# Performance work log

Measured on AMD Instinct MI355X. Metric: run time of the kernel, lower is better.

The kernel has to match this reference:

```python
import jax, jax.numpy as jnp
import numpy as np

NB = 8  # num_blocks

def setup_inputs() -> dict:
    key = jax.random.key(0)
    ks = jax.random.split(key, 8)
    C = 128
    C8 = C // 8
    s = 0.05
    x = jax.random.normal(ks[0], (1, C, 64, 64, 64), dtype=jnp.float32)
    Wq = jax.random.normal(ks[1], (C8, C), dtype=jnp.float32) * s
    bq = jax.random.normal(ks[2], (C8,), dtype=jnp.float32) * s
    Wk = jax.random.normal(ks[3], (C8, C), dtype=jnp.float32) * s
    bk = jax.random.normal(ks[4], (C8,), dtype=jnp.float32) * s
    Wv = jax.random.normal(ks[5], (C, C), dtype=jnp.float32) * s
    bv = jax.random.normal(ks[6], (C,), dtype=jnp.float32) * s
    # torch inits gamma=0 (output == x, zero grads through attention);
    # use 0.5 so the attention path is actually exercised.
    gamma = jnp.full((1,), 0.5, dtype=jnp.float32)
    return dict(x=x, Wq=Wq, bq=bq, Wk=Wk, bk=bk, Wv=Wv, bv=bv, gamma=gamma)

def reference(x, Wq, bq, Wk, bk, Wv, bv, gamma):
    B, C, D, H, W = x.shape
    db, hb, wb = D // NB, H // NB, W // NB
    n = db * hb * wb
    # (i, j, k, B, C, db, hb, wb) block layout
    xr = x.reshape(B, C, NB, db, NB, hb, NB, wb).transpose(2, 4, 6, 0, 1, 3, 5, 7)
    ar = jnp.arange(NB)
    # NOTE: original code computes k = i % num_blocks, i.e. k == i always.
    # Only the (i, j, i) diagonal blocks are attended; the rest stay zero in `out`.
    blk = xr[ar, :, ar].reshape(NB * NB * B, C, n)  # (P, C, n), P = NB*NB*B
    # 1x1x1 convs == per-voxel linear layers over channels
    q = jnp.einsum('pcn,dc->pdn', blk, Wq) + bq[None, :, None]  # (P, C/8, n)
    k = jnp.einsum('pcn,dc->pdn', blk, Wk) + bk[None, :, None]  # (P, C/8, n)
    v = jnp.einsum('pcn,dc->pdn', blk, Wv) + bv[None, :, None]  # (P, C,   n)
    attn = jax.nn.softmax(jnp.einsum('pdn,pdm->pnm', q, k), axis=-1)  # (P, n_q, n_k)
    ob = jnp.einsum('pdm,pnm->pdn', v, attn)  # value @ attn^T, (P, C, n)
    ob = ob.reshape(NB, NB, B, C, db, hb, wb)
    out = jnp.zeros_like(xr).at[ar, :, ar].set(ob)  # only k==i diagonal filled
    out = out.transpose(3, 4, 0, 5, 1, 6, 2, 7).reshape(B, C, D, H, W)
    return gamma * out + x
```

## Files before the change

kernel.cpp:

```cpp
#include <hip/hip_runtime.h>

typedef __attribute__((ext_vector_type(8))) short bf16x8;
typedef __attribute__((ext_vector_type(4))) float f32x4;
typedef __attribute__((ext_vector_type(4))) int i32x4;
typedef __attribute__((ext_vector_type(4))) float float4v;

#define MFMA16(a, b, c) __builtin_amdgcn_mfma_f32_16x16x32_bf16((a), (b), (c), 0, 0, 0)

__device__ __forceinline__ unsigned short f2bf(float f) {
    unsigned u = __builtin_bit_cast(unsigned, f);
    u += 0x7fffu + ((u >> 16) & 1u);
    return (unsigned short)(u >> 16);
}
__device__ __forceinline__ float bf2f(unsigned short s) {
    unsigned u = ((unsigned)s) << 16;
    return __builtin_bit_cast(float, u);
}
__device__ __forceinline__ int pkbf(float a, float b) {
    return (int)f2bf(a) | ((int)f2bf(b) << 16);
}

#define KOFF 131072
#define LOFF 147456

__global__ __launch_bounds__(512, 2) void battn_kernel(
    const float* __restrict__ x,
    const float* __restrict__ Wq, const float* __restrict__ bq,
    const float* __restrict__ Wk, const float* __restrict__ bk,
    const float* __restrict__ Wv, const float* __restrict__ bv,
    const float* __restrict__ gamma, float* __restrict__ out)
{
    __shared__ __attribute__((aligned(128))) char smem[147968];
    const int tid = threadIdx.x;
    const int bid = blockIdx.x;
    const int p  = ((bid & 7) << 3) | (bid >> 5);
    const int qq = (bid >> 3) & 3;
    const int ib = p >> 3, jb = p & 7;
    const int vbase = ib * 8 * 4096 + jb * 8 * 64 + ib * 8;
    const int lane = tid & 63, wv = tid >> 6;
    const int g = lane >> 4, c15 = lane & 15;

    #pragma unroll
    for (int b = 0; b < 4; ++b) {
        float4v t[8];
        #pragma unroll
        for (int j = 0; j < 8; ++j) {
            int ch = (b * 8 + j) * 512 + tid;
            int c = ch >> 7;
            int m = (ch & 127) * 4;
            int vox = ((m >> 6) << 12) + (((m >> 3) & 7) << 6) + (m & 7);
            t[j] = *(const float4v*)(x + c * 262144 + vbase + vox);
        }
        #pragma unroll
        for (int j = 0; j < 8; ++j) {
            int ch = (b * 8 + j) * 512 + tid;
            int c = ch >> 7;
            int m = (ch & 127) * 4;
            char* bp = smem + ((m * 256 + 2 * c) ^ (((m >> 2) & 7) << 4));
            *(unsigned short*)(bp)       = f2bf(t[j][0]);
            *(unsigned short*)(bp + 256) = f2bf(t[j][1]);
            *(unsigned short*)(bp + 512) = f2bf(t[j][2]);
            *(unsigned short*)(bp + 768) = f2bf(t[j][3]);
        }
    }

    bf16x8 wqf[4], wkf[4], wvf[4];
    #pragma unroll
    for (int ks = 0; ks < 4; ++ks) {
        const float4v* sq = (const float4v*)(Wq + c15 * 128 + ks * 32 + g * 8);
        const float4v* sk = (const float4v*)(Wk + c15 * 128 + ks * 32 + g * 8);
        const float4v* sv = (const float4v*)(Wv + (wv * 16 + c15) * 128 + ks * 32 + g * 8);
        float4v q0 = sq[0], q1 = sq[1];
        float4v k0 = sk[0], k1 = sk[1];
        float4v v0 = sv[0], v1 = sv[1];
        #pragma unroll
        for (int e = 0; e < 4; ++e) {
            wqf[ks][e] = (short)f2bf(q0[e]); wqf[ks][4 + e] = (short)f2bf(q1[e]);
            wkf[ks][e] = (short)f2bf(k0[e]); wkf[ks][4 + e] = (short)f2bf(k1[e]);
            wvf[ks][e] = (short)f2bf(v0[e]); wvf[ks][4 + e] = (short)f2bf(v1[e]);
        }
    }
    const float bqv = bq[c15], bkv = bk[c15];
    const f32x4 zacc = {0.f, 0.f, 0.f, 0.f};
    const bf16x8 zfrag = (bf16x8)(short)0;

    __syncthreads();

    {
        f32x4 acc = zacc;
        int mrow = qq * 128 + wv * 16 + c15;
        int sw = ((mrow >> 2) & 7) << 4;
        #pragma unroll
        for (int ks = 0; ks < 4; ++ks) {
            bf16x8 af = *(const bf16x8*)(smem + ((mrow * 256 + ks * 64 + g * 16) ^ sw));
            acc = MFMA16(af, wqf[ks], acc);
        }
        #pragma unroll
        for (int r = 0; r < 4; ++r)
            *(unsigned short*)(smem + KOFF + wv * 2048 + (g * 4 + r) * 32 + 2 * c15) = f2bf(acc[r] + bqv);
    }
    bf16x8 qf = zfrag;
    if (g < 2) qf = *(const bf16x8*)(smem + KOFF + wv * 2048 + c15 * 32 + g * 16);

    #pragma unroll
    for (int qi = 0; qi < 4; ++qi) {
        f32x4 acc = zacc;
        int mrow = wv * 64 + qi * 16 + c15;
        int sw = ((mrow >> 2) & 7) << 4;
        #pragma unroll
        for (int ks = 0; ks < 4; ++ks) {
            bf16x8 af = *(const bf16x8*)(smem + ((mrow * 256 + ks * 64 + g * 16) ^ sw));
            acc = MFMA16(af, wkf[ks], acc);
        }
        #pragma unroll
        for (int r = 0; r < 4; ++r) {
            int mk = wv * 64 + qi * 16 + g * 4 + r;
            *(unsigned short*)(smem + KOFF + mk * 32 + 2 * c15) = f2bf(acc[r] + bkv);
        }
    }

    for (int ck = 0; ck < 4; ++ck) {
        f32x4 vacc[8];
        #pragma unroll
        for (int mt = 0; mt < 8; ++mt) {
            vacc[mt] = zacc;
            int mrow = ck * 128 + mt * 16 + c15;
            int sw = ((mrow >> 2) & 7) << 4;
            #pragma unroll
            for (int ks = 0; ks < 4; ++ks) {
                bf16x8 bf = *(const bf16x8*)(smem + ((mrow * 256 + ks * 64 + g * 16) ^ sw));
                vacc[mt] = MFMA16(wvf[ks], bf, vacc[mt]);
            }
        }
        __syncthreads();
        #pragma unroll
        for (int mt = 0; mt < 8; ++mt) {
            #pragma unroll
            for (int r = 0; r < 4; ++r) {
                int c_out = wv * 16 + g * 4 + r;
                int mkl = mt * 16 + c15;
                *(unsigned short*)(smem + ck * 32768 + c_out * 256 +
                                   ((2 * mkl) ^ ((c_out & 7) << 4))) = f2bf(vacc[mt][r]);
            }
        }
    }
    __syncthreads();

    f32x4 o[8];
    #pragma unroll
    for (int ci = 0; ci < 8; ++ci) o[ci] = zacc;
    float lsum = 0.f;

    for (int kt = 0; kt < 16; ++kt) {
        int mk0 = kt * 32;
        bf16x8 ka[2];
        #pragma unroll
        for (int ki = 0; ki < 2; ++ki) {
            bf16x8 v = zfrag;
            if (g < 2) v = *(const bf16x8*)(smem + KOFF + (mk0 + ki * 16 + c15) * 32 + g * 16);
            ka[ki] = v;
        }

        f32x4 s0 = MFMA16(ka[0], qf, zacc);
        f32x4 s1 = MFMA16(ka[1], qf, zacc);
        float e00 = __expf(s0[0]), e01 = __expf(s0[1]), e02 = __expf(s0[2]), e03 = __expf(s0[3]);
        float e10 = __expf(s1[0]), e11 = __expf(s1[1]), e12 = __expf(s1[2]), e13 = __expf(s1[3]);
        lsum += (e00 + e01) + (e02 + e03) + ((e10 + e11) + (e12 + e13));
        int wA0 = pkbf(e00, e01), wB0 = pkbf(e02, e03);
        int wA1 = pkbf(e10, e11), wB1 = pkbf(e12, e13);
        int src1 = ((2 * g) & 3) * 16 + c15;
        int src2 = ((2 * g + 1) & 3) * 16 + c15;
        int sA0a = __shfl(wA0, src1, 64), sA1a = __shfl(wA1, src1, 64);
        int sB0a = __shfl(wB0, src1, 64), sB1a = __shfl(wB1, src1, 64);
        int sA0b = __shfl(wA0, src2, 64), sA1b = __shfl(wA1, src2, 64);
        int sB0b = __shfl(wB0, src2, 64), sB1b = __shfl(wB1, src2, 64);
        bool k1 = (g >= 2);
        i32x4 uu = { k1 ? sA1a : sA0a, k1 ? sB1a : sB0a,
                     k1 ? sA1b : sA0b, k1 ? sB1b : sB0b };
        bf16x8 pa = __builtin_bit_cast(bf16x8, uu);

        int ckbase = (mk0 >> 7) * 32768;
        int mklb = (2 * (mk0 & 127)) + 16 * g;
        #pragma unroll
        for (int ci = 0; ci < 8; ++ci) {
            int c = ci * 16 + c15;
            bf16x8 vb = *(const bf16x8*)(smem + ckbase + c * 256 + (mklb ^ ((c & 7) << 4)));
            o[ci] = MFMA16(pa, vb, o[ci]);
        }
    }

    {
        float l = lsum;
        l += __shfl_xor(l, 16, 64);
        l += __shfl_xor(l, 32, 64);
        if (g == 0)
            *(float*)(smem + LOFF + (wv * 16 + c15) * 4) = l;
    }

    __syncthreads();

    #pragma unroll
    for (int ci = 0; ci < 8; ++ci)
        #pragma unroll
        for (int r = 0; r < 4; ++r) {
            int nql = wv * 16 + g * 4 + r;
            int c = ci * 16 + c15;
            *(unsigned short*)(smem + c * 256 + ((2 * nql) ^ ((c & 7) << 4))) = f2bf(o[ci][r]);
        }
    __syncthreads();

    float gma = gamma[0];
    int q128 = tid & 127;
    int cb = tid >> 7;
    float invl = 1.0f / *(const float*)(smem + LOFF + q128 * 4);
    int nq = qq * 128 + q128;
    int vox = ((nq >> 6) << 12) + (((nq >> 3) & 7) << 6) + (nq & 7);
    int go = vbase + vox;
    #pragma unroll
    for (int b = 0; b < 4; ++b) {
        float xv[8];
        #pragma unroll
        for (int j = 0; j < 8; ++j) {
            int c = cb * 32 + b * 8 + j;
            xv[j] = x[c * 262144 + go];
        }
        #pragma unroll
        for (int j = 0; j < 8; ++j) {
            int c = cb * 32 + b * 8 + j;
            float ov = bf2f(*(const unsigned short*)(smem + c * 256 + ((2 * q128) ^ ((c & 7) << 4))));
            out[c * 262144 + go] = gma * (ov * invl + bv[c]) + xv[j];
        }
    }
}

extern "C" void kernel_launch(void* const* d_in, const int* in_sizes, int n_in,
                              void* d_out, int out_size, void* d_ws, size_t ws_size,
                              hipStream_t stream) {
    const float* x     = (const float*)d_in[0];
    const float* Wq    = (const float*)d_in[1];
    const float* bq    = (const float*)d_in[2];
    const float* Wk    = (const float*)d_in[3];
    const float* bk    = (const float*)d_in[4];
    const float* Wv    = (const float*)d_in[5];
    const float* bv    = (const float*)d_in[6];
    const float* gamma = (const float*)d_in[7];
    float* out = (float*)d_out;
    (void)in_sizes; (void)n_in; (void)out_size; (void)d_ws; (void)ws_size;

    hipMemcpyAsync(out, x, (size_t)out_size * sizeof(float),
                   hipMemcpyDeviceToDevice, stream);
    battn_kernel<<<dim3(256), dim3(512), 0, stream>>>(x, Wq, bq, Wk, bk, Wv, bv, gamma, out);
}
```

Measured before the change: 101.1 us.

## Pre-gather diagonal blocks into contiguous workspace before attention kernel

Adds a separate gather kernel that copies the strided diagonal 8x8x8 voxel blocks of x into a contiguous per-block workspace layout. The attention kernel then reads its input tile and residual values from that workspace with coalesced vector loads instead of scattered strided reads. The trade-off is an extra kernel launch and an extra round trip of the gathered data through memory. Each attention block re-reads its tile four times (once per query quarter), so cheaper reads may outweigh the added traffic.

New measurement: 123.8 us. 22.4% more time.

```diff
diff --git a/kernel.cpp b/kernel.cpp
--- a/kernel.cpp
+++ b/kernel.cpp
@@ -20,11 +20,29 @@
     return (int)f2bf(a) | ((int)f2bf(b) << 16);
 }
 
+__global__ __launch_bounds__(512) void gather_kernel(
+    const float* __restrict__ x, float* __restrict__ ws)
+{
+    int gid = blockIdx.x * 512 + threadIdx.x;
+    int gm = gid & 63;
+    int c  = (gid >> 6) & 127;
+    int p  = gid >> 13;
+    int ib = p >> 3, jb = p & 7;
+    int dd = gm >> 3, hh = gm & 7;
+    const float* src = x + c * 262144 + ib * 32768 + jb * 512 + ib * 8
+                         + dd * 4096 + hh * 64;
+    float4v a0 = *(const float4v*)(src);
+    float4v a1 = *(const float4v*)(src + 4);
+    float* dst = ws + (size_t)gid * 8;
+    *(float4v*)(dst)     = a0;
+    *(float4v*)(dst + 4) = a1;
+}
+
 #define KOFF 131072
 #define LOFF 147456
 
 __global__ __launch_bounds__(512, 2) void battn_kernel(
-    const float* __restrict__ x,
+    const float* __restrict__ ws,
     const float* __restrict__ Wq, const float* __restrict__ bq,
     const float* __restrict__ Wk, const float* __restrict__ bk,
     const float* __restrict__ Wv, const float* __restrict__ bv,
@@ -39,23 +57,19 @@
     const int vbase = ib * 8 * 4096 + jb * 8 * 64 + ib * 8;
     const int lane = tid & 63, wv = tid >> 6;
     const int g = lane >> 4, c15 = lane & 15;
+    const float4v* __restrict__ wsp4 = (const float4v*)(ws + p * 65536);
 
     #pragma unroll
     for (int b = 0; b < 4; ++b) {
         float4v t[8];
         #pragma unroll
+        for (int j = 0; j < 8; ++j)
+            t[j] = wsp4[(b * 8 + j) * 512 + tid];
+        #pragma unroll
         for (int j = 0; j < 8; ++j) {
-            int ch = (b * 8 + j) * 512 + tid;
-            int c = ch >> 7;
-            int m = (ch & 127) * 4;
-            int vox = ((m >> 6) << 12) + (((m >> 3) & 7) << 6) + (m & 7);
-            t[j] = *(const float4v*)(x + c * 262144 + vbase + vox);
-        }
-        #pragma unroll
-        for (int j = 0; j < 8; ++j) {
-            int ch = (b * 8 + j) * 512 + tid;
-            int c = ch >> 7;
-            int m = (ch & 127) * 4;
+            int u = (b * 8 + j) * 512 + tid;
+            int c = u >> 7;
+            int m = (u & 127) * 4;
             char* bp = smem + ((m * 256 + 2 * c) ^ (((m >> 2) & 7) << 4));
             *(unsigned short*)(bp)       = f2bf(t[j][0]);
             *(unsigned short*)(bp + 256) = f2bf(t[j][1]);
@@ -216,13 +230,14 @@
     int nq = qq * 128 + q128;
     int vox = ((nq >> 6) << 12) + (((nq >> 3) & 7) << 6) + (nq & 7);
     int go = vbase + vox;
+    const float* wsr = ws + p * 65536 + nq;
     #pragma unroll
     for (int b = 0; b < 4; ++b) {
         float xv[8];
         #pragma unroll
         for (int j = 0; j < 8; ++j) {
             int c = cb * 32 + b * 8 + j;
-            xv[j] = x[c * 262144 + go];
+            xv[j] = wsr[c * 512];
         }
         #pragma unroll
         for (int j = 0; j < 8; ++j) {
@@ -245,9 +260,11 @@
     const float* bv    = (const float*)d_in[6];
     const float* gamma = (const float*)d_in[7];
     float* out = (float*)d_out;
-    (void)in_sizes; (void)n_in; (void)out_size; (void)d_ws; (void)ws_size;
+    float* ws  = (float*)d_ws;
+    (void)in_sizes; (void)n_in; (void)out_size; (void)ws_size;
 
     hipMemcpyAsync(out, x, (size_t)out_size * sizeof(float),
                    hipMemcpyDeviceToDevice, stream);
-    battn_kernel<<<dim3(256), dim3(512), 0, stream>>>(x, Wq, bq, Wk, bk, Wv, bv, gamma, out);
-}
+    gather_kernel<<<dim3(1024), dim3(512), 0, stream>>>(x, ws);
+    battn_kernel<<<dim3(256), dim3(512), 0, stream>>>(ws, Wq, bq, Wk, bk, Wv, bv, gamma, out);
+}
```

## Split projection into separate kernel writing Q/K/V to workspace

Applied to the files above, without the earlier changes.

The fused kernel made each of the four query-quarter blocks redundantly recompute the full K and V projections for its attention block. A new proj_kernel computes Q, K and V once per block, split across 8 CTAs, and writes them as bf16 to the workspace along with a contiguous fp32 copy of x. The attention kernel then loads precomputed K and V into shared memory and reads the residual from the contiguous copy. This removes redundant MFMA work and raises parallelism in the projection phase, at the cost of an extra launch and extra workspace traffic.

New measurement: 115.7 us. 1.14x slower.

```diff
diff --git a/kernel.cpp b/kernel.cpp
--- a/kernel.cpp
+++ b/kernel.cpp
@@ -1,6 +1,7 @@
 #include <hip/hip_runtime.h>
 
 typedef __attribute__((ext_vector_type(8))) short bf16x8;
+typedef __attribute__((ext_vector_type(8))) unsigned short u16x8;
 typedef __attribute__((ext_vector_type(4))) float f32x4;
 typedef __attribute__((ext_vector_type(4))) int i32x4;
 typedef __attribute__((ext_vector_type(4))) float float4v;
@@ -20,15 +21,149 @@
     return (int)f2bf(a) | ((int)f2bf(b) << 16);
 }
 
-#define KOFF 131072
-#define LOFF 147456
-
-__global__ __launch_bounds__(512, 2) void battn_kernel(
+
+__global__ __launch_bounds__(256, 4) void proj_kernel(
     const float* __restrict__ x,
     const float* __restrict__ Wq, const float* __restrict__ bq,
     const float* __restrict__ Wk, const float* __restrict__ bk,
-    const float* __restrict__ Wv, const float* __restrict__ bv,
-    const float* __restrict__ gamma, float* __restrict__ out)
+    const float* __restrict__ Wv,
+    float* __restrict__ ws)
+{
+    __shared__ __attribute__((aligned(128))) char smem[36864];
+    const int tid = threadIdx.x;
+    const int bid = blockIdx.x;
+    const int p = bid >> 3, s = bid & 7;
+    const int ib = p >> 3, jb = p & 7;
+    const int vbase = ib * 32768 + jb * 512 + ib * 8;
+    const int lane = tid & 63, wv = tid >> 6;
+    const int g = lane >> 4, c15 = lane & 15;
+    const f32x4 zacc = {0.f, 0.f, 0.f, 0.f};
+
+    bf16x8 wqf[4], wkf[4], wvf2[2][4];
+    #pragma unroll
+    for (int ks = 0; ks < 4; ++ks) {
+        const float4v* sq = (const float4v*)(Wq + c15 * 128 + ks * 32 + g * 8);
+        const float4v* sk = (const float4v*)(Wk + c15 * 128 + ks * 32 + g * 8);
+        float4v q0 = sq[0], q1 = sq[1];
+        float4v k0 = sk[0], k1 = sk[1];
+        #pragma unroll
+        for (int e = 0; e < 4; ++e) {
+            wqf[ks][e] = (short)f2bf(q0[e]); wqf[ks][4 + e] = (short)f2bf(q1[e]);
+            wkf[ks][e] = (short)f2bf(k0[e]); wkf[ks][4 + e] = (short)f2bf(k1[e]);
+        }
+        #pragma unroll
+        for (int cg = 0; cg < 2; ++cg) {
+            const float4v* sv = (const float4v*)(Wv + (wv * 32 + cg * 16 + c15) * 128 + ks * 32 + g * 8);
+            float4v v0 = sv[0], v1 = sv[1];
+            #pragma unroll
+            for (int e = 0; e < 4; ++e) {
+                wvf2[cg][ks][e] = (short)f2bf(v0[e]); wvf2[cg][ks][4 + e] = (short)f2bf(v1[e]);
+            }
+        }
+    }
+    const float bqv = bq[c15], bkv = bk[c15];
+
+    float* blkws = ws + p * 65536;
+    #pragma unroll
+    for (int k = 0; k < 2; ++k) {
+        int pi = k * 256 + tid;
+        int cpair = pi >> 3, m8 = pi & 7;
+        int c0 = cpair * 2;
+        int mg = s * 64 + m8 * 8;
+        int vox = s * 4096 + m8 * 64;
+        const float* src0 = x + c0 * 262144 + vbase + vox;
+        float4v a0 = *(const float4v*)(src0);
+        float4v a1 = *(const float4v*)(src0 + 4);
+        float4v b0 = *(const float4v*)(src0 + 262144);
+        float4v b1 = *(const float4v*)(src0 + 262144 + 4);
+        *(float4v*)(blkws + c0 * 512 + mg)           = a0;
+        *(float4v*)(blkws + c0 * 512 + mg + 4)       = a1;
+        *(float4v*)(blkws + c0 * 512 + 512 + mg)     = b0;
+        *(float4v*)(blkws + c0 * 512 + 512 + mg + 4) = b1;
+        int ml = m8 * 8;
+        #pragma unroll
+        for (int j = 0; j < 4; ++j) {
+            int m = ml + j;
+            unsigned v = (unsigned)f2bf(a0[j]) | ((unsigned)f2bf(b0[j]) << 16);
+            *(unsigned*)(smem + ((m * 256 + 4 * cpair) ^ (((m >> 2) & 7) << 4))) = v;
+        }
+        #pragma unroll
+        for (int j = 0; j < 4; ++j) {
+            int m = ml + 4 + j;
+            unsigned v = (unsigned)f2bf(a1[j]) | ((unsigned)f2bf(b1[j]) << 16);
+            *(unsigned*)(smem + ((m * 256 + 4 * cpair) ^ (((m >> 2) & 7) << 4))) = v;
+        }
+    }
+    __syncthreads();
+
+    {
+        f32x4 qa = zacc, kacc = zacc;
+        int mrow = wv * 16 + c15;
+        int sw = ((mrow >> 2) & 7) << 4;
+        #pragma unroll
+        for (int ks = 0; ks < 4; ++ks) {
+            bf16x8 af = *(const bf16x8*)(smem + ((mrow * 256 + ks * 64 + g * 16) ^ sw));
+            qa = MFMA16(af, wqf[ks], qa);
+            kacc = MFMA16(af, wkf[ks], kacc);
+        }
+        #pragma unroll
+        for (int r = 0; r < 4; ++r) {
+            int row = wv * 16 + g * 4 + r;
+            *(unsigned short*)(smem + 16384 + row * 32 + 2 * c15) = f2bf(qa[r] + bqv);
+            *(unsigned short*)(smem + 18432 + row * 32 + 2 * c15) = f2bf(kacc[r] + bkv);
+        }
+    }
+
+    f32x4 vacc[2][4];
+    #pragma unroll
+    for (int cg = 0; cg < 2; ++cg)
+        #pragma unroll
+        for (int mt = 0; mt < 4; ++mt) {
+            vacc[cg][mt] = zacc;
+            int mrow = mt * 16 + c15;
+            int sw = ((mrow >> 2) & 7) << 4;
+            #pragma unroll
+            for (int ks = 0; ks < 4; ++ks) {
+                bf16x8 bf = *(const bf16x8*)(smem + ((mrow * 256 + ks * 64 + g * 16) ^ sw));
+                vacc[cg][mt] = MFMA16(wvf2[cg][ks], bf, vacc[cg][mt]);
+            }
+        }
+    char* vt = smem + 20480 + wv * 4096;
+    #pragma unroll
+    for (int cg = 0; cg < 2; ++cg)
+        #pragma unroll
+        for (int mt = 0; mt < 4; ++mt)
+            #pragma unroll
+            for (int r = 0; r < 4; ++r)
+                *(unsigned short*)(vt + (cg * 16 + g * 4 + r) * 128 + 2 * (mt * 16 + c15))
+                    = f2bf(vacc[cg][mt][r]);
+
+    unsigned short* wsh = (unsigned short*)(ws + 4194304);
+    unsigned short* wsv = wsh + 1048576 + p * 65536 + s * 64;
+    #pragma unroll
+    for (int i = 0; i < 4; ++i) {
+        int lb = i * 1024 + lane * 16;
+        u16x8 vv = *(const u16x8*)(vt + lb);
+        int c_local = lb >> 7;
+        int moff = (lane & 7) * 8;
+        *(u16x8*)(wsv + (wv * 32 + c_local) * 512 + moff) = vv;
+    }
+    __syncthreads();
+    unsigned short* wsq = wsh + p * 8192 + s * 1024;
+    unsigned short* wsk = wsh + 524288 + p * 8192 + s * 1024;
+    long long qd = *(const long long*)(smem + 16384 + tid * 8);
+    long long kd = *(const long long*)(smem + 18432 + tid * 8);
+    *(long long*)(wsq + tid * 4) = qd;
+    *(long long*)(wsk + tid * 4) = kd;
+}
+
+#define KOFF 131072
+#define LOFF 147456
+
+__global__ __launch_bounds__(512, 2) void attn_kernel(
+    const float* __restrict__ ws,
+    const float* __restrict__ bv, const float* __restrict__ gamma,
+    float* __restrict__ out)
 {
     __shared__ __attribute__((aligned(128))) char smem[147968];
     const int tid = threadIdx.x;
@@ -36,114 +171,32 @@
     const int p  = ((bid & 7) << 3) | (bid >> 5);
     const int qq = (bid >> 3) & 3;
     const int ib = p >> 3, jb = p & 7;
-    const int vbase = ib * 8 * 4096 + jb * 8 * 64 + ib * 8;
+    const int vbase = ib * 32768 + jb * 512 + ib * 8;
     const int lane = tid & 63, wv = tid >> 6;
     const int g = lane >> 4, c15 = lane & 15;
-
-    #pragma unroll
-    for (int b = 0; b < 4; ++b) {
-        float4v t[8];
-        #pragma unroll
-        for (int j = 0; j < 8; ++j) {
-            int ch = (b * 8 + j) * 512 + tid;
-            int c = ch >> 7;
-            int m = (ch & 127) * 4;
-            int vox = ((m >> 6) << 12) + (((m >> 3) & 7) << 6) + (m & 7);
-            t[j] = *(const float4v*)(x + c * 262144 + vbase + vox);
-        }
-        #pragma unroll
-        for (int j = 0; j < 8; ++j) {
-            int ch = (b * 8 + j) * 512 + tid;
-            int c = ch >> 7;
-            int m = (ch & 127) * 4;
-            char* bp = smem + ((m * 256 + 2 * c) ^ (((m >> 2) & 7) << 4));
-            *(unsigned short*)(bp)       = f2bf(t[j][0]);
-            *(unsigned short*)(bp + 256) = f2bf(t[j][1]);
-            *(unsigned short*)(bp + 512) = f2bf(t[j][2]);
-            *(unsigned short*)(bp + 768) = f2bf(t[j][3]);
-        }
-    }
-
-    bf16x8 wqf[4], wkf[4], wvf[4];
-    #pragma unroll
-    for (int ks = 0; ks < 4; ++ks) {
-        const float4v* sq = (const float4v*)(Wq + c15 * 128 + ks * 32 + g * 8);
-        const float4v* sk = (const float4v*)(Wk + c15 * 128 + ks * 32 + g * 8);
-        const float4v* sv = (const float4v*)(Wv + (wv * 16 + c15) * 128 + ks * 32 + g * 8);
-        float4v q0 = sq[0], q1 = sq[1];
-        float4v k0 = sk[0], k1 = sk[1];
-        float4v v0 = sv[0], v1 = sv[1];
-        #pragma unroll
-        for (int e = 0; e < 4; ++e) {
-            wqf[ks][e] = (short)f2bf(q0[e]); wqf[ks][4 + e] = (short)f2bf(q1[e]);
-            wkf[ks][e] = (short)f2bf(k0[e]); wkf[ks][4 + e] = (short)f2bf(k1[e]);
-            wvf[ks][e] = (short)f2bf(v0[e]); wvf[ks][4 + e] = (short)f2bf(v1[e]);
-        }
-    }
-    const float bqv = bq[c15], bkv = bk[c15];
     const f32x4 zacc = {0.f, 0.f, 0.f, 0.f};
     const bf16x8 zfrag = (bf16x8)(short)0;
 
-    __syncthreads();
-
-    {
-        f32x4 acc = zacc;
-        int mrow = qq * 128 + wv * 16 + c15;
-        int sw = ((mrow >> 2) & 7) << 4;
-        #pragma unroll
-        for (int ks = 0; ks < 4; ++ks) {
-            bf16x8 af = *(const bf16x8*)(smem + ((mrow * 256 + ks * 64 + g * 16) ^ sw));
-            acc = MFMA16(af, wqf[ks], acc);
-        }
-        #pragma unroll
-        for (int r = 0; r < 4; ++r)
-            *(unsigned short*)(smem + KOFF + wv * 2048 + (g * 4 + r) * 32 + 2 * c15) = f2bf(acc[r] + bqv);
+    const unsigned short* wsh = (const unsigned short*)(ws + 4194304);
+    const unsigned short* wsq = wsh + p * 8192;
+    const unsigned short* wsk = wsh + 524288 + p * 8192;
+    const unsigned short* wsv = wsh + 1048576 + p * 65536;
+
+    #pragma unroll
+    for (int i = 0; i < 16; ++i) {
+        int li = (i * 512 + tid) * 8;
+        int c = li >> 9, m = li & 511;
+        u16x8 v = *(const u16x8*)(wsv + li);
+        *(u16x8*)(smem + c * 1024 + ((2 * m) ^ ((c & 7) << 4))) = v;
+    }
+    #pragma unroll
+    for (int i = 0; i < 2; ++i) {
+        int t8 = i * 512 + tid;
+        u16x8 v = *(const u16x8*)(wsk + t8 * 8);
+        *(u16x8*)(smem + KOFF + t8 * 16) = v;
     }
     bf16x8 qf = zfrag;
-    if (g < 2) qf = *(const bf16x8*)(smem + KOFF + wv * 2048 + c15 * 32 + g * 16);
-
-    #pragma unroll
-    for (int qi = 0; qi < 4; ++qi) {
-        f32x4 acc = zacc;
-        int mrow = wv * 64 + qi * 16 + c15;
-        int sw = ((mrow >> 2) & 7) << 4;
-        #pragma unroll
-        for (int ks = 0; ks < 4; ++ks) {
-            bf16x8 af = *(const bf16x8*)(smem + ((mrow * 256 + ks * 64 + g * 16) ^ sw));
-            acc = MFMA16(af, wkf[ks], acc);
-        }
-        #pragma unroll
-        for (int r = 0; r < 4; ++r) {
-            int mk = wv * 64 + qi * 16 + g * 4 + r;
-            *(unsigned short*)(smem + KOFF + mk * 32 + 2 * c15) = f2bf(acc[r] + bkv);
-        }
-    }
-
-    for (int ck = 0; ck < 4; ++ck) {
-        f32x4 vacc[8];
-        #pragma unroll
-        for (int mt = 0; mt < 8; ++mt) {
-            vacc[mt] = zacc;
-            int mrow = ck * 128 + mt * 16 + c15;
-            int sw = ((mrow >> 2) & 7) << 4;
-            #pragma unroll
-            for (int ks = 0; ks < 4; ++ks) {
-                bf16x8 bf = *(const bf16x8*)(smem + ((mrow * 256 + ks * 64 + g * 16) ^ sw));
-                vacc[mt] = MFMA16(wvf[ks], bf, vacc[mt]);
-            }
-        }
-        __syncthreads();
-        #pragma unroll
-        for (int mt = 0; mt < 8; ++mt) {
-            #pragma unroll
-            for (int r = 0; r < 4; ++r) {
-                int c_out = wv * 16 + g * 4 + r;
-                int mkl = mt * 16 + c15;
-                *(unsigned short*)(smem + ck * 32768 + c_out * 256 +
-                                   ((2 * mkl) ^ ((c_out & 7) << 4))) = f2bf(vacc[mt][r]);
-            }
-        }
-    }
+    if (g < 2) qf = *(const bf16x8*)(wsq + (qq * 128 + wv * 16 + c15) * 16 + g * 8);
     __syncthreads();
 
     f32x4 o[8];
@@ -179,12 +232,10 @@
                      k1 ? sA1b : sA0b, k1 ? sB1b : sB0b };
         bf16x8 pa = __builtin_bit_cast(bf16x8, uu);
 
-        int ckbase = (mk0 >> 7) * 32768;
-        int mklb = (2 * (mk0 & 127)) + 16 * g;
         #pragma unroll
         for (int ci = 0; ci < 8; ++ci) {
             int c = ci * 16 + c15;
-            bf16x8 vb = *(const bf16x8*)(smem + ckbase + c * 256 + (mklb ^ ((c & 7) << 4)));
+            bf16x8 vb = *(const bf16x8*)(smem + c * 1024 + ((2 * mk0 + 16 * g) ^ ((c & 7) << 4)));
             o[ci] = MFMA16(pa, vb, o[ci]);
         }
     }
@@ -216,13 +267,14 @@
     int nq = qq * 128 + q128;
     int vox = ((nq >> 6) << 12) + (((nq >> 3) & 7) << 6) + (nq & 7);
     int go = vbase + vox;
+    const float* blkws = ws + p * 65536 + nq;
     #pragma unroll
     for (int b = 0; b < 4; ++b) {
         float xv[8];
         #pragma unroll
         for (int j = 0; j < 8; ++j) {
             int c = cb * 32 + b * 8 + j;
-            xv[j] = x[c * 262144 + go];
+            xv[j] = blkws[c * 512];
         }
         #pragma unroll
         for (int j = 0; j < 8; ++j) {
@@ -245,9 +297,11 @@
     const float* bv    = (const float*)d_in[6];
     const float* gamma = (const float*)d_in[7];
     float* out = (float*)d_out;
-    (void)in_sizes; (void)n_in; (void)out_size; (void)d_ws; (void)ws_size;
+    float* ws  = (float*)d_ws;
+    (void)in_sizes; (void)n_in; (void)out_size; (void)ws_size;
 
     hipMemcpyAsync(out, x, (size_t)out_size * sizeof(float),
                    hipMemcpyDeviceToDevice, stream);
-    battn_kernel<<<dim3(256), dim3(512), 0, stream>>>(x, Wq, bq, Wk, bk, Wv, bv, gamma, out);
-}
+    proj_kernel<<<dim3(512), dim3(256), 0, stream>>>(x, Wq, bq, Wk, bk, Wv, ws);
+    attn_kernel<<<dim3(256), dim3(512), 0, stream>>>(ws, bv, gamma, out);
+}
```
